# Kernel optimization log

Hardware: AMD Instinct MI355X
Metric: run time of the kernel (lower is better)

## Reference

```python
import jax, jax.numpy as jnp
import numpy as np

INF = 10000.0


def setup_inputs() -> dict:
    key = jax.random.key(0)
    ks = jax.random.split(key, 4)
    bs, seqlen, hidden = 8, 512, 768
    head_size, heads = 64, 12
    inputs = jax.random.normal(ks[0], (bs, seqlen, hidden), dtype=jnp.float32)
    attention_mask = jnp.ones((bs, seqlen), dtype=jnp.int32)
    W1 = jax.random.normal(ks[1], (hidden, head_size * 2), dtype=jnp.float32) * 0.02
    b1 = jnp.zeros((head_size * 2,), dtype=jnp.float32)
    W2 = jax.random.normal(ks[2], (head_size * 2, heads * 2), dtype=jnp.float32) * 0.02
    b2 = jnp.zeros((heads * 2,), dtype=jnp.float32)
    return {"inputs": inputs, "attention_mask": attention_mask,
            "W1": W1, "b1": b1, "W2": W2, "b2": b2}


def _rope(t, sin, cos):
    # t: [b, s, d]; sin/cos: [s, d//2]
    t1, t2 = t[..., 0::2], t[..., 1::2]
    return jnp.stack([t1 * cos - t2 * sin, t1 * sin + t2 * cos], axis=-1).reshape(t.shape)


def reference(inputs, attention_mask, W1, b1, W2, b2):
    bs, seqlen = inputs.shape[:2]
    head_size = W1.shape[1] // 2
    x = inputs @ W1 + b1                      # [b, s, 2*head_size]
    qw, kw = x[..., 0::2], x[..., 1::2]       # [b, s, head_size] each
    # rotary embedding (computed like the buffer in the torch module)
    pos = jnp.arange(seqlen, dtype=jnp.float32)
    inv_freq = 1.0 / (10000.0 ** (jnp.arange(0, head_size, 2, dtype=jnp.float32) / head_size))
    freqs = pos[:, None] * inv_freq[None, :]  # [s, head_size//2]
    sin, cos = jnp.sin(freqs), jnp.cos(freqs)
    qw = _rope(qw, sin, cos)
    kw = _rope(kw, sin, cos)
    logits = jnp.einsum('bmd,bnd->bmn', qw, kw) / (head_size ** 0.5)  # [b, s, s]
    bias = (x @ W2 + b2).transpose(0, 2, 1) / 2.0                      # [b, 2*heads, s]
    logits = logits[:, None] + bias[:, ::2, None, :] + bias[:, 1::2, :, None]  # [b, h, s, s]
    am = attention_mask.astype(logits.dtype)
    mask = 1.0 - am[:, None, None, :] * am[:, None, :, None]           # [b, 1, s, s]
    logits = logits - mask * INF
    # tril mask: positions with end < start (j < i)
    idx = jnp.arange(seqlen)
    tril = (idx[None, :] < idx[:, None]).astype(logits.dtype)[None, None]  # [1, 1, s, s]
    logits = logits - tril * INF
    mask_out = jnp.logical_or(mask.astype(bool),
                              jnp.broadcast_to(tril.astype(bool), (bs, 1, seqlen, seqlen)))
    return logits, mask_out
```

## Files before the change

kernel.cpp:

```cpp
#include <hip/hip_runtime.h>

#define BSZ 8
#define SEQ 512
#define HID 768
#define N1 128
#define N2 24
#define HS 64
#define HEADS 12
#define INFV 10000.0f

typedef __attribute__((ext_vector_type(8))) short s8b;
typedef __attribute__((ext_vector_type(4))) float f32x4;

__device__ __forceinline__ unsigned short f2bf(float f) {
    union { float f; unsigned int u; } c; c.f = f;
    unsigned int u = c.u;
    u += 0x7FFFu + ((u >> 16) & 1u);
    return (unsigned short)(u >> 16);
}

__device__ __forceinline__ s8b loadB(const float* __restrict__ wsrc) {
    union { s8b v; unsigned short u[8]; } r;
#pragma unroll
    for (int i = 0; i < 8; ++i) r.u[i] = f2bf(wsrc[i * N1]);
    return r.v;
}

#define ASLOT(chunk, r) (((chunk) * 16 + ((r) ^ ((chunk) & 7))) * 8)

__global__ __launch_bounds__(512, 4) void k1_proj(
    const float* __restrict__ inp, const float* __restrict__ W1,
    const float* __restrict__ b1, const float* __restrict__ W2,
    const float* __restrict__ b2,
    float* __restrict__ qw, float* __restrict__ kwT,
    float* __restrict__ bP0, float* __restrict__ bP1)
{
    __shared__ unsigned short aF[96 * 16 * 8];
    __shared__ float ps[16][64];
    __shared__ float xs[16][72];
    __shared__ float kT[32][17];

    const int tid = threadIdx.x;
    const int rt = blockIdx.x >> 1;
    const int ch = blockIdx.x & 1;
    const int row0 = rt * 16;
    const int b = row0 >> 9;
    const int m0 = row0 & 511;

    {
        const float4* src = (const float4*)(inp + (size_t)row0 * HID);
#pragma unroll
        for (int i = 0; i < 6; ++i) {
            int f4 = tid + i * 512;
            int r = f4 / 192;
            int c4 = f4 % 192;
            float4 v = src[f4];
            int chunk = c4 >> 1;
            int half = c4 & 1;
            ushort4 w;
            w.x = f2bf(v.x); w.y = f2bf(v.y); w.z = f2bf(v.z); w.w = f2bf(v.w);
            *(ushort4*)&aF[ASLOT(chunk, r) + half * 4] = w;
        }
    }
    __syncthreads();

    const int wv = tid >> 6;
    const int ln = tid & 63;
    const int lr = ln & 15;
    const int lg = ln >> 4;
    const int w3 = wv & 3;
    const int kh = wv >> 2;
    const int cg = ch * 64 + w3 * 16 + lr;

    const float* wbase = W1 + (size_t)(kh * 384 + lg * 8) * N1 + cg;

    f32x4 acc = {0.f, 0.f, 0.f, 0.f};
    s8b bA = loadB(wbase);
    s8b bB = loadB(wbase + 32 * N1);

#define AFRAG(kc) (*(const s8b*)&aF[ASLOT((kh * 12 + (kc)) * 4 + lg, lr)])
#pragma unroll
    for (int kc = 0; kc < 12; kc += 2) {
        acc = __builtin_amdgcn_mfma_f32_16x16x32_bf16(AFRAG(kc), bA, acc, 0, 0, 0);
        if (kc + 2 < 12) bA = loadB(wbase + (size_t)(kc + 2) * 32 * N1);
        acc = __builtin_amdgcn_mfma_f32_16x16x32_bf16(AFRAG(kc + 1), bB, acc, 0, 0, 0);
        if (kc + 3 < 12) bB = loadB(wbase + (size_t)(kc + 3) * 32 * N1);
    }
#undef AFRAG

    if (kh == 1) {
#pragma unroll
        for (int g = 0; g < 4; ++g) ps[lg * 4 + g][w3 * 16 + lr] = acc[g];
    }
    __syncthreads();
    if (kh == 0) {
        float b1v = b1[cg];
#pragma unroll
        for (int g = 0; g < 4; ++g)
            xs[lg * 4 + g][w3 * 16 + lr] = acc[g] + ps[lg * 4 + g][w3 * 16 + lr] + b1v;
    }
    __syncthreads();

    if (tid < 16 * N2) {
        int r = tid / N2, c = tid - r * N2;
        const float* w2p = W2 + (size_t)(ch * 64) * N2 + c;
        float dot = (ch == 0) ? b2[c] : 0.0f;
#pragma unroll 8
        for (int kl = 0; kl < 64; ++kl)
            dot = fmaf(xs[r][kl], w2p[kl * N2], dot);
        float* bP = ch ? bP1 : bP0;
        bP[(size_t)(b * N2 + c) * SEQ + m0 + r] = dot * 0.5f;
    }

    if (tid < 256) {
        const int r = tid >> 4, jj = tid & 15;
        const int j = ch * 16 + jj;
        const int m = m0 + r;
        const float C = 0.4152410118609203f;
        float invf = exp2f(-(float)j * C);
        float ang = (float)m * invf;
        float sv = __sinf(ang), cv = __cosf(ang);
        float4 xv = *(const float4*)&xs[r][4 * jj];
        float rq0 = xv.x * cv - xv.z * sv;
        float rq1 = xv.x * sv + xv.z * cv;
        float rk0 = xv.y * cv - xv.w * sv;
        float rk1 = xv.y * sv + xv.w * cv;
        *(float2*)(qw + (size_t)(b * SEQ + m) * HS + 2 * j) = make_float2(rq0, rq1);
        kT[2 * jj][r]     = rk0;
        kT[2 * jj + 1][r] = rk1;
    }
    __syncthreads();

    if (tid < 256) {
        int dl = tid >> 3, q = tid & 7;
        float2 v = *(const float2*)&kT[dl][2 * q];
        *(float2*)(kwT + (size_t)(b * HS + ch * 32 + dl) * SEQ + m0 + 2 * q) = v;
    }
}

__global__ __launch_bounds__(256) void k2_out(
    const float* __restrict__ qw, const float* __restrict__ kwT,
    const float* __restrict__ bP0, const float* __restrict__ bP1,
    const int* __restrict__ am, float* __restrict__ out)
{
    __shared__ float q_lds[8][HS];
    __shared__ float bo[8][HEADS];
    __shared__ int amm[8];

    const int tid = threadIdx.x;
    const int b = blockIdx.x >> 6;
    const int m0 = (blockIdx.x & 63) * 8;

#pragma unroll
    for (int i = 0; i < 2; ++i) {
        int idx = tid + i * 256;
        q_lds[idx >> 6][idx & 63] = qw[(size_t)(b * SEQ + m0) * HS + idx];
    }
    if (tid < 96) {
        int r = tid / 12, h = tid - r * 12;
        size_t ix = (size_t)(b * N2 + 2 * h + 1) * SEQ + m0 + r;
        bo[r][h] = bP0[ix] + bP1[ix];
    }
    if (tid < 8) amm[tid] = am[b * SEQ + m0 + tid];
    __syncthreads();

    const int g = tid >> 7;
    const int n0 = (tid & 127) * 4;

    float4 qk[4] = {{0,0,0,0},{0,0,0,0},{0,0,0,0},{0,0,0,0}};

#pragma unroll
    for (int d0 = 0; d0 < HS; d0 += 8) {
        float4 kn[8];
#pragma unroll
        for (int dd = 0; dd < 8; ++dd)
            kn[dd] = *(const float4*)&kwT[(size_t)(b * HS + d0 + dd) * SEQ + n0];
#pragma unroll
        for (int r = 0; r < 4; ++r) {
            float4 qa = *(const float4*)&q_lds[g * 4 + r][d0];
            float4 qb = *(const float4*)&q_lds[g * 4 + r][d0 + 4];
#pragma unroll
            for (int c = 0; c < 4; ++c) {
                float* k0 = (float*)&kn[0];
            }
            qk[r].x = fmaf(qa.x, kn[0].x, qk[r].x); qk[r].y = fmaf(qa.x, kn[0].y, qk[r].y);
            qk[r].z = fmaf(qa.x, kn[0].z, qk[r].z); qk[r].w = fmaf(qa.x, kn[0].w, qk[r].w);
            qk[r].x = fmaf(qa.y, kn[1].x, qk[r].x); qk[r].y = fmaf(qa.y, kn[1].y, qk[r].y);
            qk[r].z = fmaf(qa.y, kn[1].z, qk[r].z); qk[r].w = fmaf(qa.y, kn[1].w, qk[r].w);
            qk[r].x = fmaf(qa.z, kn[2].x, qk[r].x); qk[r].y = fmaf(qa.z, kn[2].y, qk[r].y);
            qk[r].z = fmaf(qa.z, kn[2].z, qk[r].z); qk[r].w = fmaf(qa.z, kn[2].w, qk[r].w);
            qk[r].x = fmaf(qa.w, kn[3].x, qk[r].x); qk[r].y = fmaf(qa.w, kn[3].y, qk[r].y);
            qk[r].z = fmaf(qa.w, kn[3].z, qk[r].z); qk[r].w = fmaf(qa.w, kn[3].w, qk[r].w);
            qk[r].x = fmaf(qb.x, kn[4].x, qk[r].x); qk[r].y = fmaf(qb.x, kn[4].y, qk[r].y);
            qk[r].z = fmaf(qb.x, kn[4].z, qk[r].z); qk[r].w = fmaf(qb.x, kn[4].w, qk[r].w);
            qk[r].x = fmaf(qb.y, kn[5].x, qk[r].x); qk[r].y = fmaf(qb.y, kn[5].y, qk[r].y);
            qk[r].z = fmaf(qb.y, kn[5].z, qk[r].z); qk[r].w = fmaf(qb.y, kn[5].w, qk[r].w);
            qk[r].x = fmaf(qb.z, kn[6].x, qk[r].x); qk[r].y = fmaf(qb.z, kn[6].y, qk[r].y);
            qk[r].z = fmaf(qb.z, kn[6].z, qk[r].z); qk[r].w = fmaf(qb.z, kn[6].w, qk[r].w);
            qk[r].x = fmaf(qb.w, kn[7].x, qk[r].x); qk[r].y = fmaf(qb.w, kn[7].y, qk[r].y);
            qk[r].z = fmaf(qb.w, kn[7].z, qk[r].z); qk[r].w = fmaf(qb.w, kn[7].w, qk[r].w);
        }
    }

    int4 amn = *(const int4*)&am[b * SEQ + n0];
    float4 pen[4], mo[4];
#pragma unroll
    for (int r = 0; r < 4; ++r) {
        int m = m0 + g * 4 + r;
        int a = amm[g * 4 + r];
        pen[r].x = (1.0f - (float)(amn.x * a)) * INFV + ((n0 + 0 < m) ? INFV : 0.0f);
        pen[r].y = (1.0f - (float)(amn.y * a)) * INFV + ((n0 + 1 < m) ? INFV : 0.0f);
        pen[r].z = (1.0f - (float)(amn.z * a)) * INFV + ((n0 + 2 < m) ? INFV : 0.0f);
        pen[r].w = (1.0f - (float)(amn.w * a)) * INFV + ((n0 + 3 < m) ? INFV : 0.0f);
        mo[r].x = ((amn.x * a != 1) || (n0 + 0 < m)) ? 1.0f : 0.0f;
        mo[r].y = ((amn.y * a != 1) || (n0 + 1 < m)) ? 1.0f : 0.0f;
        mo[r].z = ((amn.z * a != 1) || (n0 + 2 < m)) ? 1.0f : 0.0f;
        mo[r].w = ((amn.w * a != 1) || (n0 + 3 < m)) ? 1.0f : 0.0f;
    }

    const size_t obase = (size_t)b * HEADS * SEQ * SEQ + n0;
#pragma unroll
    for (int h = 0; h < HEADS; ++h) {
        size_t ix = (size_t)(b * N2 + 2 * h) * SEQ + n0;
        float4 e0 = *(const float4*)&bP0[ix];
        float4 e1 = *(const float4*)&bP1[ix];
        float4 be = {e0.x + e1.x, e0.y + e1.y, e0.z + e1.z, e0.w + e1.w};
#pragma unroll
        for (int r = 0; r < 4; ++r) {
            float bos = bo[g * 4 + r][h];
            float4 v;
            v.x = fmaf(qk[r].x, 0.125f, be.x + bos) - pen[r].x;
            v.y = fmaf(qk[r].y, 0.125f, be.y + bos) - pen[r].y;
            v.z = fmaf(qk[r].z, 0.125f, be.z + bos) - pen[r].z;
            v.w = fmaf(qk[r].w, 0.125f, be.w + bos) - pen[r].w;
            *(float4*)&out[obase + ((size_t)h * SEQ + m0 + g * 4 + r) * SEQ] = v;
        }
    }
    const size_t mbase = (size_t)BSZ * HEADS * SEQ * SEQ
                       + ((size_t)b * SEQ + m0 + g * 4) * SEQ + n0;
#pragma unroll
    for (int r = 0; r < 4; ++r)
        *(float4*)&out[mbase + (size_t)r * SEQ] = mo[r];
}

extern "C" void kernel_launch(void* const* d_in, const int* in_sizes, int n_in,
                              void* d_out, int out_size, void* d_ws, size_t ws_size,
                              hipStream_t stream) {
    const float* inp = (const float*)d_in[0];
    const int*   am  = (const int*)d_in[1];
    const float* W1  = (const float*)d_in[2];
    const float* b1  = (const float*)d_in[3];
    const float* W2  = (const float*)d_in[4];
    const float* b2  = (const float*)d_in[5];

    float* ws    = (float*)d_ws;
    float* qw    = ws;
    float* kwT   = ws + 262144;
    float* bP0   = ws + 524288;
    float* bP1   = ws + 622592;

    float* out = (float*)d_out;

    hipLaunchKernelGGL(k1_proj, dim3(512), dim3(512), 0, stream,
                       inp, W1, b1, W2, b2, qw, kwT, bP0, bP1);
    hipLaunchKernelGGL(k2_out, dim3(512), dim3(256), 0, stream,
                       qw, kwT, bP0, bP1, am, out);
}
```

Measured before the change: 40.62 us.

## Pre-convert W1 to transposed bf16 and compute full 128 columns per block

Adds a small pre-kernel that converts W1 to bf16 in a transposed layout so k1 can load B fragments as 16-byte vectors instead of eight strided scalar loads with per-element conversion. k1 now handles all 128 output columns per 16-row tile with 8 waves each covering the full K=768. This removes the K-split partial-sum exchange and the two-buffer bias split, so k2 reads a single bias array. The cost is an extra kernel launch and fewer k1 blocks (256 instead of 512) with higher register use from holding 24 B fragments.

```diff
diff --git a/kernel.cpp b/kernel.cpp
--- a/kernel.cpp
+++ b/kernel.cpp
@@ -19,33 +19,47 @@
     return (unsigned short)(u >> 16);
 }
 
-__device__ __forceinline__ s8b loadB(const float* __restrict__ wsrc) {
-    union { s8b v; unsigned short u[8]; } r;
-#pragma unroll
-    for (int i = 0; i < 8; ++i) r.u[i] = f2bf(wsrc[i * N1]);
-    return r.v;
+__global__ __launch_bounds__(128) void k0_w1t(const float* __restrict__ W1,
+                                              unsigned short* __restrict__ W1T) {
+    const int c = threadIdx.x;
+    const int k0 = blockIdx.x * 8;
+    unsigned short v[8];
+#pragma unroll
+    for (int i = 0; i < 8; ++i)
+        v[i] = f2bf(W1[(size_t)(k0 + i) * N1 + c]);
+    unsigned short* dst = W1T + (size_t)c * HID + k0;
+#pragma unroll
+    for (int i = 0; i < 8; ++i) dst[i] = v[i];
 }
 
 #define ASLOT(chunk, r) (((chunk) * 16 + ((r) ^ ((chunk) & 7))) * 8)
 
-__global__ __launch_bounds__(512, 4) void k1_proj(
-    const float* __restrict__ inp, const float* __restrict__ W1,
+__global__ __launch_bounds__(512, 2) void k1_proj(
+    const float* __restrict__ inp, const unsigned short* __restrict__ W1T,
     const float* __restrict__ b1, const float* __restrict__ W2,
     const float* __restrict__ b2,
     float* __restrict__ qw, float* __restrict__ kwT,
-    float* __restrict__ bP0, float* __restrict__ bP1)
+    float* __restrict__ bias)
 {
     __shared__ unsigned short aF[96 * 16 * 8];
-    __shared__ float ps[16][64];
-    __shared__ float xs[16][72];
-    __shared__ float kT[32][17];
+    __shared__ float xs[16][132];
+    __shared__ float kT[64][17];
 
     const int tid = threadIdx.x;
-    const int rt = blockIdx.x >> 1;
-    const int ch = blockIdx.x & 1;
-    const int row0 = rt * 16;
+    const int row0 = blockIdx.x * 16;
     const int b = row0 >> 9;
     const int m0 = row0 & 511;
+
+    const int wv = tid >> 6;
+    const int ln = tid & 63;
+    const int lr = ln & 15;
+    const int lg = ln >> 4;
+    const int cg = wv * 16 + lr;
+
+    const s8b* bp = (const s8b*)W1T + ((size_t)cg * 96 + lg);
+    s8b bfr[24];
+#pragma unroll
+    for (int kc = 0; kc < 24; ++kc) bfr[kc] = bp[kc * 4];
 
     {
         const float4* src = (const float4*)(inp + (size_t)row0 * HID);
@@ -64,84 +78,60 @@
     }
     __syncthreads();
 
-    const int wv = tid >> 6;
-    const int ln = tid & 63;
-    const int lr = ln & 15;
-    const int lg = ln >> 4;
-    const int w3 = wv & 3;
-    const int kh = wv >> 2;
-    const int cg = ch * 64 + w3 * 16 + lr;
-
-    const float* wbase = W1 + (size_t)(kh * 384 + lg * 8) * N1 + cg;
-
     f32x4 acc = {0.f, 0.f, 0.f, 0.f};
-    s8b bA = loadB(wbase);
-    s8b bB = loadB(wbase + 32 * N1);
-
-#define AFRAG(kc) (*(const s8b*)&aF[ASLOT((kh * 12 + (kc)) * 4 + lg, lr)])
-#pragma unroll
-    for (int kc = 0; kc < 12; kc += 2) {
-        acc = __builtin_amdgcn_mfma_f32_16x16x32_bf16(AFRAG(kc), bA, acc, 0, 0, 0);
-        if (kc + 2 < 12) bA = loadB(wbase + (size_t)(kc + 2) * 32 * N1);
-        acc = __builtin_amdgcn_mfma_f32_16x16x32_bf16(AFRAG(kc + 1), bB, acc, 0, 0, 0);
-        if (kc + 3 < 12) bB = loadB(wbase + (size_t)(kc + 3) * 32 * N1);
-    }
-#undef AFRAG
-
-    if (kh == 1) {
-#pragma unroll
-        for (int g = 0; g < 4; ++g) ps[lg * 4 + g][w3 * 16 + lr] = acc[g];
-    }
-    __syncthreads();
-    if (kh == 0) {
+#pragma unroll
+    for (int kc = 0; kc < 24; ++kc) {
+        s8b a = *(const s8b*)&aF[ASLOT(kc * 4 + lg, lr)];
+        acc = __builtin_amdgcn_mfma_f32_16x16x32_bf16(a, bfr[kc], acc, 0, 0, 0);
+    }
+
+    {
         float b1v = b1[cg];
 #pragma unroll
         for (int g = 0; g < 4; ++g)
-            xs[lg * 4 + g][w3 * 16 + lr] = acc[g] + ps[lg * 4 + g][w3 * 16 + lr] + b1v;
+            xs[lg * 4 + g][cg] = acc[g] + b1v;
     }
     __syncthreads();
 
     if (tid < 16 * N2) {
         int r = tid / N2, c = tid - r * N2;
-        const float* w2p = W2 + (size_t)(ch * 64) * N2 + c;
-        float dot = (ch == 0) ? b2[c] : 0.0f;
+        const float* w2p = W2 + c;
+        float dot = b2[c];
 #pragma unroll 8
-        for (int kl = 0; kl < 64; ++kl)
-            dot = fmaf(xs[r][kl], w2p[kl * N2], dot);
-        float* bP = ch ? bP1 : bP0;
-        bP[(size_t)(b * N2 + c) * SEQ + m0 + r] = dot * 0.5f;
-    }
-
-    if (tid < 256) {
-        const int r = tid >> 4, jj = tid & 15;
-        const int j = ch * 16 + jj;
+        for (int kl = 0; kl < N1; ++kl)
+            dot = fmaf(xs[r][kl], w2p[(size_t)kl * N2], dot);
+        bias[(size_t)(b * N2 + c) * SEQ + m0 + r] = dot * 0.5f;
+    }
+
+    {
+        const int r = tid >> 5, j = tid & 31;
         const int m = m0 + r;
         const float C = 0.4152410118609203f;
         float invf = exp2f(-(float)j * C);
         float ang = (float)m * invf;
         float sv = __sinf(ang), cv = __cosf(ang);
-        float4 xv = *(const float4*)&xs[r][4 * jj];
+        float4 xv = *(const float4*)&xs[r][4 * j];
         float rq0 = xv.x * cv - xv.z * sv;
         float rq1 = xv.x * sv + xv.z * cv;
         float rk0 = xv.y * cv - xv.w * sv;
         float rk1 = xv.y * sv + xv.w * cv;
         *(float2*)(qw + (size_t)(b * SEQ + m) * HS + 2 * j) = make_float2(rq0, rq1);
-        kT[2 * jj][r]     = rk0;
-        kT[2 * jj + 1][r] = rk1;
-    }
-    __syncthreads();
-
-    if (tid < 256) {
-        int dl = tid >> 3, q = tid & 7;
-        float2 v = *(const float2*)&kT[dl][2 * q];
-        *(float2*)(kwT + (size_t)(b * HS + ch * 32 + dl) * SEQ + m0 + 2 * q) = v;
+        kT[2 * j][r]     = rk0;
+        kT[2 * j + 1][r] = rk1;
+    }
+    __syncthreads();
+
+    {
+        int d = tid >> 3, q = tid & 7;
+        float2 v = *(const float2*)&kT[d][2 * q];
+        *(float2*)(kwT + (size_t)(b * HS + d) * SEQ + m0 + 2 * q) = v;
     }
 }
 
 __global__ __launch_bounds__(256) void k2_out(
     const float* __restrict__ qw, const float* __restrict__ kwT,
-    const float* __restrict__ bP0, const float* __restrict__ bP1,
-    const int* __restrict__ am, float* __restrict__ out)
+    const float* __restrict__ bias, const int* __restrict__ am,
+    float* __restrict__ out)
 {
     __shared__ float q_lds[8][HS];
     __shared__ float bo[8][HEADS];
@@ -158,8 +148,7 @@
     }
     if (tid < 96) {
         int r = tid / 12, h = tid - r * 12;
-        size_t ix = (size_t)(b * N2 + 2 * h + 1) * SEQ + m0 + r;
-        bo[r][h] = bP0[ix] + bP1[ix];
+        bo[r][h] = bias[(size_t)(b * N2 + 2 * h + 1) * SEQ + m0 + r];
     }
     if (tid < 8) amm[tid] = am[b * SEQ + m0 + tid];
     __syncthreads();
@@ -179,10 +168,6 @@
         for (int r = 0; r < 4; ++r) {
             float4 qa = *(const float4*)&q_lds[g * 4 + r][d0];
             float4 qb = *(const float4*)&q_lds[g * 4 + r][d0 + 4];
-#pragma unroll
-            for (int c = 0; c < 4; ++c) {
-                float* k0 = (float*)&kn[0];
-            }
             qk[r].x = fmaf(qa.x, kn[0].x, qk[r].x); qk[r].y = fmaf(qa.x, kn[0].y, qk[r].y);
             qk[r].z = fmaf(qa.x, kn[0].z, qk[r].z); qk[r].w = fmaf(qa.x, kn[0].w, qk[r].w);
             qk[r].x = fmaf(qa.y, kn[1].x, qk[r].x); qk[r].y = fmaf(qa.y, kn[1].y, qk[r].y);
@@ -221,10 +206,7 @@
     const size_t obase = (size_t)b * HEADS * SEQ * SEQ + n0;
 #pragma unroll
     for (int h = 0; h < HEADS; ++h) {
-        size_t ix = (size_t)(b * N2 + 2 * h) * SEQ + n0;
-        float4 e0 = *(const float4*)&bP0[ix];
-        float4 e1 = *(const float4*)&bP1[ix];
-        float4 be = {e0.x + e1.x, e0.y + e1.y, e0.z + e1.z, e0.w + e1.w};
+        float4 be = *(const float4*)&bias[(size_t)(b * N2 + 2 * h) * SEQ + n0];
 #pragma unroll
         for (int r = 0; r < 4; ++r) {
             float bos = bo[g * 4 + r][h];
@@ -256,13 +238,14 @@
     float* ws    = (float*)d_ws;
     float* qw    = ws;
     float* kwT   = ws + 262144;
-    float* bP0   = ws + 524288;
-    float* bP1   = ws + 622592;
+    float* bias  = ws + 524288;
+    unsigned short* W1T = (unsigned short*)(ws + 622592);
 
     float* out = (float*)d_out;
 
-    hipLaunchKernelGGL(k1_proj, dim3(512), dim3(512), 0, stream,
-                       inp, W1, b1, W2, b2, qw, kwT, bP0, bP1);
+    hipLaunchKernelGGL(k0_w1t, dim3(96), dim3(128), 0, stream, W1, W1T);
+    hipLaunchKernelGGL(k1_proj, dim3(256), dim3(512), 0, stream,
+                       inp, W1T, b1, W2, b2, qw, kwT, bias);
     hipLaunchKernelGGL(k2_out, dim3(512), dim3(256), 0, stream,
-                       qw, kwT, bP0, bP1, am, out);
-}
+                       qw, kwT, bias, am, out);
+}
```

Measured after the change: 46.03 us. 13.3% more time.
